# Kernel optimization log

Hardware: AMD Instinct MI355X
Metric: run time of the kernel (lower is better)

Reference implementation:

```python
import jax, jax.numpy as jnp
import numpy as np

BS, S, D, N, E = 16, 8, 10, 32, 300
H, STATE_DIM, MID, OC = 128, 96, 256, 100

def setup_inputs():
    ks = jax.random.split(jax.random.key(0), 24)
    g = lambda i, shape: (0.02 * jax.random.normal(ks[i], shape)).astype(jnp.float32)
    return {
        "stock_news": jax.random.normal(ks[0], (BS, S, D, N, E), dtype=jnp.float32),
        "stock_feats": jax.random.normal(ks[1], (BS, STATE_DIM), dtype=jnp.float32),
        "conv_w3": g(2, (S, OC, E, 3)), "conv_b3": g(3, (S, OC)),
        "conv_w4": g(4, (S, OC, E, 4)), "conv_b4": g(5, (S, OC)),
        "conv_w5": g(6, (S, OC, E, 5)), "conv_b5": g(7, (S, OC)),
        "w_ih": g(8, (S, 4 * H, 3 * OC)), "w_hh": g(9, (S, 4 * H, H)),
        "b_ih": g(10, (S, 4 * H)), "b_hh": g(11, (S, 4 * H)),
        "linX_w": g(12, (S, H, 2 * H)), "linX_b": g(13, (S, H)),
        "linY_w": g(14, (S, 64, H)), "linY_b": g(15, (S, 64)),
        "w1": g(16, (24, STATE_DIM)), "b1": g(17, (24,)),
        "w2": g(18, (16, 24)), "b2": g(19, (16,)),
        "arch_w1": g(20, (MID, 16 + 64 * S)), "arch_b1": g(21, (MID,)),
        "arch_w2": g(22, (S, MID)), "arch_b2": g(23, (S,)),
        "action_var": jnp.full((S,), -0.25, dtype=jnp.float32),
    }

def _conv_maxpool(x, w, b, k):
    # x: [S,B,D,N,E], w: [S,OC,E,k] -> conv1d over news axis then max-pool -> [S,B,D,OC]
    L = x.shape[3] - k + 1
    y = jnp.broadcast_to(b[:, None, None, None, :], (x.shape[0], x.shape[1], x.shape[2], L, w.shape[1]))
    for j in range(k):
        y = y + jnp.einsum('sbdne,soe->sbdno', x[:, :, :, j:j + L, :], w[:, :, :, j])
    return y.max(axis=3)

def _lstm_attn(xs, w_ih, w_hh, b_ih, b_hh):
    # single-stock LSTM (batch_first) + attention from original code; xs: [B,D,I] -> [B,2H]
    pre = jnp.einsum('bdi,gi->dbg', xs, w_ih) + b_ih + b_hh  # [D,B,4H]
    h0 = jnp.zeros((xs.shape[0], w_hh.shape[1]), xs.dtype)
    def step(carry, g_t):
        h, c = carry
        gates = g_t + h @ w_hh.T
        i, f, g, o = jnp.split(gates, 4, axis=-1)  # PyTorch gate order i,f,g,o
        c = jax.nn.sigmoid(f) * c + jax.nn.sigmoid(i) * jnp.tanh(g)
        h = jax.nn.sigmoid(o) * jnp.tanh(c)
        return (h, c), h
    (hn, _), outs = jax.lax.scan(step, (h0, h0), pre)
    outs = outs.transpose(1, 0, 2)  # [B,D,H]
    w = jnp.einsum('bh,bdh->bd', hn, outs)[:, None, :]  # [B,1,D]
    w = jax.nn.softmax(w, axis=1)  # softmax over singleton dim, exactly as torch code (yields ones)
    out = jnp.sum(w.transpose(0, 2, 1) * outs, axis=1)  # [B,H]
    return jnp.concatenate([hn, out], axis=-1)  # [B,2H]

def _forward(stock_news, stock_feats, conv_w3, conv_b3, conv_w4, conv_b4, conv_w5, conv_b5,
             w_ih, w_hh, b_ih, b_hh, linX_w, linX_b, linY_w, linY_b,
             w1, b1, w2, b2, arch_w1, arch_b1, arch_w2, arch_b2, action_var):
    x = stock_news.transpose(1, 0, 2, 3, 4)  # [S,B,D,N,E]
    feats = [_conv_maxpool(x, w, b, k) for (w, b, k) in
             ((conv_w3, conv_b3, 3), (conv_w4, conv_b4, 4), (conv_w5, conv_b5, 5))]
    text = jnp.concatenate(feats, axis=-1)  # [S,B,D,300]
    comb = jax.vmap(_lstm_attn)(text, w_ih, w_hh, b_ih, b_hh)  # [S,B,2H]
    hX = jax.nn.relu(jnp.einsum('sbi,shi->sbh', comb, linX_w) + linX_b[:, None, :])  # dropout is eval-mode identity
    hY = jax.nn.relu(jnp.einsum('sbh,soh->sbo', hX, linY_w) + linY_b[:, None, :])  # [S,B,64]
    stock_text = hY.transpose(1, 0, 2).reshape(stock_news.shape[0], -1)  # [B,S*64]
    f = jax.nn.relu(stock_feats @ w1.T + b1) @ w2.T + b2  # [B,16]
    total = jnp.concatenate([stock_text, f], axis=-1)  # [B,16+64S]
    mu = jnp.tanh(jax.nn.relu(total @ arch_w1.T + arch_b1) @ arch_w2.T + arch_b2)
    return mu, jnp.exp(action_var)

def reference(stock_news, stock_feats, conv_w3, conv_b3, conv_w4, conv_b4, conv_w5, conv_b5,
              w_ih, w_hh, b_ih, b_hh, linX_w, linX_b, linY_w, linY_b,
              w1, b1, w2, b2, arch_w1, arch_b1, arch_w2, arch_b2, action_var):
    return _forward(stock_news, stock_feats, conv_w3, conv_b3, conv_w4, conv_b4, conv_w5, conv_b5,
                    w_ih, w_hh, b_ih, b_hh, linX_w, linX_b, linY_w, linY_b,
                    w1, b1, w2, b2, arch_w1, arch_b1, arch_w2, arch_b2, action_var)
```

## Files before the change

### kernel.cpp

```cpp
#include <hip/hip_runtime.h>
#include <hip/hip_fp8.h>
#include <math.h>

#define S_   8
#define B_   16
#define D_   10
#define N_   32
#define E_   300
#define H_   128
#define G4_  512
#define SDIM_ 96
#define MID_ 256
#define TOT_ 528

#define GP_  514

typedef unsigned short u16;
typedef unsigned int u32;
typedef unsigned char u8;
typedef unsigned long long u64;
typedef __attribute__((ext_vector_type(8))) short short8;
typedef __attribute__((ext_vector_type(4))) float f32x4;

static __device__ __forceinline__ u16 f2bf(float f) {
    unsigned u = __builtin_bit_cast(unsigned, f);
    return (u16)((u + 0x7FFFu + ((u >> 16) & 1u)) >> 16);
}
static __device__ __forceinline__ u8 f2fp8(float f) {
    __hip_fp8_e4m3 t(f);
    return (u8)t.__x;
}

template<int KT>
static __device__ __forceinline__ void fill_row(const float* __restrict__ src,
                                                u8* __restrict__ tilerow, int lane) {
    const float4* s4 = reinterpret_cast<const float4*>(src);
    for (int i4 = lane; i4 < 75 * KT; i4 += 64) {
        float4 v = s4[i4];
        float vv[4] = {v.x, v.y, v.z, v.w};
#pragma unroll
        for (int k = 0; k < 4; ++k) {
            int p = i4 * 4 + k;
            int e = p / KT, tap = p - e * KT;
            tilerow[tap * 300 + e] = f2fp8(vv[k] * 16.0f);
        }
    }
}

__global__ __launch_bounds__(256) void prep(
        const float* __restrict__ w3, const float* __restrict__ b3,
        const float* __restrict__ w4, const float* __restrict__ b4,
        const float* __restrict__ w5, const float* __restrict__ b5,
        const float* __restrict__ w_ih, const float* __restrict__ w_hh,
        const float* __restrict__ lxw, const float* __restrict__ lyw,
        const float* __restrict__ aw1,
        u8* __restrict__ wpack3, u16* __restrict__ wpre2,
        u16* __restrict__ whh_pk, u16* __restrict__ lxw_pk, u16* __restrict__ lyw_pk,
        float* __restrict__ bcomb, float* __restrict__ aw1T) {
    const int blk = blockIdx.x, tid = threadIdx.x;

    if (blk < 640) {
        __shared__ u8 tile4[4][1504];
        const int s = blk / 80, cq = blk % 80;
        const int c0 = cq * 4;
        const int ch4 = tid >> 6, lane = tid & 63;
        for (int i = tid; i < 1504; i += 256)
            reinterpret_cast<u32*>(&tile4[0][0])[i] = 0u;
        __syncthreads();
        const int c = c0 + ch4;
        if (cq < 25)      fill_row<3>(w3 + (size_t)((s * 100 + c      ) * 300) * 3, &tile4[ch4][0], lane);
        else if (cq < 50) fill_row<4>(w4 + (size_t)((s * 100 + c - 100) * 300) * 4, &tile4[ch4][0], lane);
        else if (cq < 75) fill_row<5>(w5 + (size_t)((s * 100 + c - 200) * 300) * 5, &tile4[ch4][0], lane);
        __syncthreads();
        u32* dst0 = reinterpret_cast<u32*>(wpack3) + (size_t)s * 120320;
        const int kss = tid >> 5, m = tid & 31;
        const int ch = m >> 3, b0 = (m & 7) * 4;
#pragma unroll
        for (int ksb = 0; ksb < 6; ++ksb) {
            int ks = ksb * 8 + kss;
            if (ks < 47) {
                int kk = ks * 32 + b0;
                u32 v = (u32)tile4[ch][kk] | ((u32)tile4[ch][kk + 1] << 8)
                      | ((u32)tile4[ch][kk + 2] << 16) | ((u32)tile4[ch][kk + 3] << 24);
                dst0[(size_t)ks * 2560 + cq * 32 + m] = v;
            }
        }
    } else if (blk < 1248) {
        __shared__ u16 tile2[16][320];
        const int ch = tid >> 4, lane = tid & 15;
        u32* dst0; int nks, slab;
        if (blk < 896) {
            int u = blk - 640, s = u >> 5, gg = u & 31;
            int g = gg * 16 + ch;
            const float4* s4 = reinterpret_cast<const float4*>(w_ih + (size_t)(s * 512 + g) * 300);
            for (int i4 = lane; i4 < 75; i4 += 16) {
                float4 v = s4[i4];
                tile2[ch][i4*4+0]=f2bf(v.x); tile2[ch][i4*4+1]=f2bf(v.y);
                tile2[ch][i4*4+2]=f2bf(v.z); tile2[ch][i4*4+3]=f2bf(v.w);
            }
            for (int p = 300 + lane; p < 320; p += 16) tile2[ch][p] = 0;
            dst0 = reinterpret_cast<u32*>(wpre2 + (size_t)s * 163840) + gg * 256;
            nks = 10; slab = 8192;
        } else if (blk < 1152) {
            int u = blk - 896, s = u >> 5, gg = u & 31;
            int g = gg * 16 + ch;
            const float4* s4 = reinterpret_cast<const float4*>(w_hh + (size_t)(s * 512 + g) * 128);
            for (int i4 = lane; i4 < 32; i4 += 16) {
                float4 v = s4[i4];
                tile2[ch][i4*4+0]=f2bf(v.x); tile2[ch][i4*4+1]=f2bf(v.y);
                tile2[ch][i4*4+2]=f2bf(v.z); tile2[ch][i4*4+3]=f2bf(v.w);
            }
            dst0 = reinterpret_cast<u32*>(whh_pk + (size_t)s * 65536) + gg * 256;
            nks = 4; slab = 8192;
        } else if (blk < 1216) {
            int u = blk - 1152, s = u >> 3, gg = u & 7;
            int g = gg * 16 + ch;
            const float4* s4 = reinterpret_cast<const float4*>(lxw + (size_t)(s * 128 + g) * 256);
            for (int i4 = lane; i4 < 64; i4 += 16) {
                float4 v = s4[i4];
                tile2[ch][i4*4+0]=f2bf(v.x); tile2[ch][i4*4+1]=f2bf(v.y);
                tile2[ch][i4*4+2]=f2bf(v.z); tile2[ch][i4*4+3]=f2bf(v.w);
            }
            dst0 = reinterpret_cast<u32*>(lxw_pk + (size_t)s * 32768) + gg * 256;
            nks = 8; slab = 2048;
        } else {
            int u = blk - 1216, s = u >> 2, gg = u & 3;
            int g = gg * 16 + ch;
            const float4* s4 = reinterpret_cast<const float4*>(lyw + (size_t)(s * 64 + g) * 128);
            for (int i4 = lane; i4 < 32; i4 += 16) {
                float4 v = s4[i4];
                tile2[ch][i4*4+0]=f2bf(v.x); tile2[ch][i4*4+1]=f2bf(v.y);
                tile2[ch][i4*4+2]=f2bf(v.z); tile2[ch][i4*4+3]=f2bf(v.w);
            }
            dst0 = reinterpret_cast<u32*>(lyw_pk + (size_t)s * 8192) + gg * 256;
            nks = 4; slab = 1024;
        }
        __syncthreads();
        const int mch = tid >> 4, rem = (tid * 2) & 31;
        for (int ks = 0; ks < nks; ++ks) {
            u32 v = (u32)tile2[mch][ks * 32 + rem] | ((u32)tile2[mch][ks * 32 + rem + 1] << 16);
            dst0[(size_t)ks * slab + tid] = v;
        }
    } else if (blk < 1384) {
        __shared__ float ldsT[32][33];
        int u = blk - 1248;
        int it = u >> 3, jt = u & 7;
        int i0 = it * 32, t0 = jt * 32;
        int ivalid = (i0 + 32 <= 528) ? 32 : (528 - i0);
        const int row = tid >> 3, cf = tid & 7;
        float4 v = make_float4(0.f, 0.f, 0.f, 0.f);
        if (cf * 4 < ivalid)
            v = *reinterpret_cast<const float4*>(aw1 + (size_t)(t0 + row) * 528 + i0 + cf * 4);
        ldsT[cf * 4 + 0][row] = v.x; ldsT[cf * 4 + 1][row] = v.y;
        ldsT[cf * 4 + 2][row] = v.z; ldsT[cf * 4 + 3][row] = v.w;
        __syncthreads();
        if (row < ivalid) {
            float4 w;
            w.x = ldsT[row][cf * 4 + 0]; w.y = ldsT[row][cf * 4 + 1];
            w.z = ldsT[row][cf * 4 + 2]; w.w = ldsT[row][cf * 4 + 3];
            *reinterpret_cast<float4*>(aw1T + (size_t)(i0 + row) * 256 + t0 + cf * 4) = w;
        }
    } else {
        for (int i = tid; i < 2560; i += 256) {
            int c = i % 320, s = i / 320;
            float bv = 0.f;
            if (c < 100)      bv = b3[s*100 + c];
            else if (c < 200) bv = b4[s*100 + c - 100];
            else if (c < 300) bv = b5[s*100 + c - 200];
            bcomb[i] = bv;
        }
    }
}

__global__ __launch_bounds__(512, 1) void conv_mfma(const float* __restrict__ news,
                                                    const u8* __restrict__ wpack3,
                                                    const float* __restrict__ bcomb,
                                                    u16* __restrict__ text_bf) {
    __shared__ u8 xs[5 * 10816];
    float* part = reinterpret_cast<float*>(xs);
    const int tid = threadIdx.x, bid = blockIdx.x;
    const int s = bid & 7, rr_ = bid >> 3, b = rr_ >> 1, half = rr_ & 1;
    const int l = tid & 63, wvi = tid >> 6;
    const int wm = wvi >> 2, wn = wvi & 3;
    const int q = l >> 4, r16 = l & 15;

    const u8* gp[5];
#pragma unroll
    for (int nt = 0; nt < 5; ++nt) {
        int c = wn * 80 + nt * 16 + r16;
        gp[nt] = wpack3 + (size_t)s * 481280 + c * 32 + q * 8;
    }

    u64 bf0[5], bf1[5];
#pragma unroll
    for (int nt = 0; nt < 5; ++nt) bf0[nt] = *reinterpret_cast<const u64*>(gp[nt]);
#pragma unroll
    for (int nt = 0; nt < 5; ++nt) bf1[nt] = *reinterpret_cast<const u64*>(gp[nt] + 10240);

    {
        const float4* xg = reinterpret_cast<const float4*>(
            news + (size_t)((b * 8 + s) * 10 + half * 5) * 9600);
        for (int base = 0; base < 12000; base += 4096) {
            float4 v[8];
#pragma unroll
            for (int j = 0; j < 8; ++j) {
                int idx = base + j * 512 + tid;
                if (idx < 12000) v[j] = xg[idx];
            }
#pragma unroll
            for (int j = 0; j < 8; ++j) {
                int idx = base + j * 512 + tid;
                if (idx < 12000) {
                    int day = idx / 2400, rem = idx - day * 2400;
                    u32 o = (u32)f2fp8(v[j].x) | ((u32)f2fp8(v[j].y) << 8)
                          | ((u32)f2fp8(v[j].z) << 16) | ((u32)f2fp8(v[j].w) << 24);
                    *reinterpret_cast<u32*>(&xs[day * 10816 + rem * 4]) = o;
                }
            }
        }
        for (int i = tid; i < 1520; i += 512) {
            int day = i / 304, p = i - day * 304;
            *reinterpret_cast<u32*>(&xs[day * 10816 + 9600 + p * 4]) = 0u;
        }
    }
    __syncthreads();

    f32x4 acc[5][5];
#pragma unroll
    for (int mt = 0; mt < 5; ++mt)
#pragma unroll
        for (int nt = 0; nt < 5; ++nt) acc[mt][nt] = (f32x4)(0.f);

#define LOADA(dst, ks) do {                                                       \
    _Pragma("unroll")                                                             \
    for (int mt_ = 0; mt_ < 5; ++mt_) {                                           \
        int di_ = wm * 5 + mt_;                                                   \
        int off_ = (di_ >> 1) * 10816 + (((di_ & 1) << 4) + r16) * 300            \
                   + (ks) * 32 + q * 8;                                           \
        u32 lo_ = *reinterpret_cast<const u32*>(&xs[off_]);                       \
        u32 hi_ = *reinterpret_cast<const u32*>(&xs[off_ + 4]);                   \
        dst[mt_] = (u64)lo_ | ((u64)hi_ << 32);                                   \
    } } while (0)

#define MFMAS(bfv, av) do {                                                       \
    _Pragma("unroll")                                                             \
    for (int nt_ = 0; nt_ < 5; ++nt_)                                             \
        _Pragma("unroll")                                                         \
        for (int mt_ = 0; mt_ < 5; ++mt_)                                         \
            acc[mt_][nt_] = __builtin_amdgcn_mfma_f32_16x16x32_fp8_fp8(          \
                (long long)av[mt_], (long long)bfv[nt_], acc[mt_][nt_], 0, 0, 0); \
    } while (0)

    for (int ks = 0; ks < 46; ks += 2) {
        u64 a0[5], a1[5];
        LOADA(a0, ks);
        MFMAS(bf0, a0);
#pragma unroll
        for (int nt = 0; nt < 5; ++nt)
            bf0[nt] = *reinterpret_cast<const u64*>(gp[nt] + (ks + 2) * 10240);

        LOADA(a1, ks + 1);
        MFMAS(bf1, a1);
        if (ks + 3 < 47) {
#pragma unroll
            for (int nt = 0; nt < 5; ++nt)
                bf1[nt] = *reinterpret_cast<const u64*>(gp[nt] + (ks + 3) * 10240);
        }
    }
    {
        u64 a0[5];
        LOADA(a0, 46);
        MFMAS(bf0, a0);
    }
#undef LOADA
#undef MFMAS

    __syncthreads();

#pragma unroll
    for (int mt = 0; mt < 5; ++mt) {
        const int di = wm * 5 + mt;
        const int nwb = (di & 1) << 4;
#pragma unroll
        for (int nt = 0; nt < 5; ++nt) {
            int oc = wn * 80 + nt * 16 + r16;
            int L = (oc < 100) ? 30 : (oc < 200) ? 29 : 28;
            float mx = -3e38f;
#pragma unroll
            for (int rr = 0; rr < 4; ++rr) {
                int nw = nwb + q * 4 + rr;
                if (nw < L) mx = fmaxf(mx, acc[mt][nt][rr]);
            }
            mx = fmaxf(mx, __shfl_xor(mx, 16));
            mx = fmaxf(mx, __shfl_xor(mx, 32));
            if (l < 16) part[di * 320 + wn * 80 + nt * 16 + l] = mx;
        }
    }
    __syncthreads();
    for (int i = tid; i < 1600; i += 512) {
        int day = i / 320, oc = i - day * 320;
        float mx = fmaxf(part[(2 * day) * 320 + oc], part[(2 * day + 1) * 320 + oc]);
        text_bf[((size_t)(s * 16 + b) * 10 + half * 5 + day) * 320 + oc] =
            f2bf(mx * 0.0625f + bcomb[s * 320 + oc]);
    }
}

__global__ __launch_bounds__(256) void lstm_pre_mfma(const u16* __restrict__ text_bf,
                                                     const u16* __restrict__ wpre2,
                                                     const float* __restrict__ b_ih,
                                                     const float* __restrict__ b_hh,
                                                     float* __restrict__ pre) {
    __shared__ u16 as16[16 * 320];
    const int blk = blockIdx.x;
    const int s = blk & 7, rest = blk >> 3;
    const int d = rest % 10, gq = rest / 10;
    const int sd = s * 10 + d;
    const int tid = threadIdx.x, l = tid & 63, w = tid >> 6, q = l >> 4, r16 = l & 15;

    for (int i = tid; i < 640; i += 256) {
        int r = i / 40, c = i % 40;
        *reinterpret_cast<float4*>(as16 + r * 320 + ((c ^ (r & 7)) << 3)) =
            *reinterpret_cast<const float4*>(text_bf + ((size_t)(s * 16 + r) * 10 + d) * 320 + c * 8);
    }
    __syncthreads();

    const u16* gpb[2];
#pragma unroll
    for (int nt = 0; nt < 2; ++nt) {
        int g = gq * 128 + w * 32 + nt * 16 + r16;
        gpb[nt] = wpre2 + (size_t)s * 163840 + g * 32 + q * 8;
    }

    f32x4 acc[2];
#pragma unroll
    for (int nt = 0; nt < 2; ++nt) acc[nt] = (f32x4)(0.f);

    for (int ks = 0; ks < 10; ++ks) {
        short8 a = *reinterpret_cast<const short8*>(
            as16 + r16 * 320 + (((ks * 4 + q) ^ (r16 & 7)) << 3));
#pragma unroll
        for (int nt = 0; nt < 2; ++nt) {
            short8 bf = *reinterpret_cast<const short8*>(gpb[nt] + ks * 16384);
            acc[nt] = __builtin_amdgcn_mfma_f32_16x16x32_bf16(a, bf, acc[nt], 0, 0, 0);
        }
    }

#pragma unroll
    for (int nt = 0; nt < 2; ++nt) {
        int g = gq * 128 + w * 32 + nt * 16 + r16;
        float bias = b_ih[s * G4_ + g] + b_hh[s * G4_ + g];
#pragma unroll
        for (int r = 0; r < 4; ++r) {
            int brow = q * 4 + r;
            pre[((size_t)sd * 16 + brow) * 512 + g] = acc[nt][r] + bias;
        }
    }
}

__global__ __launch_bounds__(512, 1) void stock_tail(const float* __restrict__ pre,
                                                     const u16* __restrict__ whh_pk,
                                                     const u16* __restrict__ lxw_pk,
                                                     const u16* __restrict__ lyw_pk,
                                                     const float* __restrict__ lxb,
                                                     const float* __restrict__ lyb,
                                                     float* __restrict__ total) {
    __shared__ float gates[16 * GP_];
    __shared__ u16 hA[16 * 128];
    __shared__ u16 combA[16 * 256];
    __shared__ u16 hxA[16 * 128];
    const int s = blockIdx.x;
    const int t = threadIdx.x, l = t & 63, wv = t >> 6, q = l >> 4, r16 = l & 15;

    short8 ghr[4][4];
#pragma unroll
    for (int ks2 = 0; ks2 < 4; ++ks2)
#pragma unroll
        for (int nt = 0; nt < 4; ++nt) {
            int g = wv * 64 + nt * 16 + r16;
            ghr[ks2][nt] = *reinterpret_cast<const short8*>(
                whh_pk + (size_t)s * 65536 + ks2 * 16384 + g * 32 + q * 8);
        }

    reinterpret_cast<u64*>(hA)[t] = 0ull;
    float cst[4] = {0.f, 0.f, 0.f, 0.f};
    float hsum[4] = {0.f, 0.f, 0.f, 0.f};

    float pc[16], pn[16];
#pragma unroll
    for (int k = 0; k < 4; ++k) {
        int p = t + 512 * k; int b = p >> 7, h = p & 127;
        const float* base = pre + ((size_t)((s * 10 + 0) * 16 + b)) * 512 + h;
#pragma unroll
        for (int g = 0; g < 4; ++g) pc[k * 4 + g] = base[g * 128];
    }
    __syncthreads();

    for (int d = 0; d < D_; ++d) {
        f32x4 acc[4];
#pragma unroll
        for (int nt = 0; nt < 4; ++nt) acc[nt] = (f32x4)(0.f);
#pragma unroll
        for (int ks2 = 0; ks2 < 4; ++ks2) {
            int gran = (ks2 * 4 + q) ^ (r16 & 7);
            short8 ah = *reinterpret_cast<const short8*>(&hA[r16 * 128 + gran * 8]);
#pragma unroll
            for (int nt = 0; nt < 4; ++nt)
                acc[nt] = __builtin_amdgcn_mfma_f32_16x16x32_bf16(ah, ghr[ks2][nt], acc[nt], 0, 0, 0);
        }
        if (d + 1 < D_) {
#pragma unroll
            for (int k = 0; k < 4; ++k) {
                int p = t + 512 * k; int b = p >> 7, h = p & 127;
                const float* base = pre + ((size_t)((s * 10 + d + 1) * 16 + b)) * 512 + h;
#pragma unroll
                for (int g = 0; g < 4; ++g) pn[k * 4 + g] = base[g * 128];
            }
        }
        __syncthreads();
#pragma unroll
        for (int nt = 0; nt < 4; ++nt) {
            int g = wv * 64 + nt * 16 + r16;
#pragma unroll
            for (int rr = 0; rr < 4; ++rr)
                gates[(q * 4 + rr) * GP_ + g] = acc[nt][rr];
        }
        __syncthreads();
#pragma unroll
        for (int k = 0; k < 4; ++k) {
            int p = t + 512 * k;
            int b = p >> 7, h = p & 127;
            float ig = 1.f / (1.f + expf(-(pc[k*4+0] + gates[b * GP_ + h])));
            float fg = 1.f / (1.f + expf(-(pc[k*4+1] + gates[b * GP_ + 128 + h])));
            float gg = tanhf(pc[k*4+2] + gates[b * GP_ + 256 + h]);
            float og = 1.f / (1.f + expf(-(pc[k*4+3] + gates[b * GP_ + 384 + h])));
            float c = fg * cst[k] + ig * gg;
            cst[k] = c;
            float hv = og * tanhf(c);
            hsum[k] += hv;
            hA[b * 128 + (((h >> 3) ^ (b & 7)) << 3) + (h & 7)] = f2bf(hv);
            if (d == D_ - 1) {
                combA[b * 256 + (((h >> 3) ^ (b & 7)) << 3) + (h & 7)] = f2bf(hv);
                combA[b * 256 + ((((128 + h) >> 3) ^ (b & 7)) << 3) + (h & 7)] = f2bf(hsum[k]);
            }
        }
#pragma unroll
        for (int i = 0; i < 16; ++i) pc[i] = pn[i];
        __syncthreads();
    }

    {
        int col = wv * 16 + r16;
        f32x4 xacc = (f32x4)(lxb[s * H_ + col]);
#pragma unroll
        for (int ks = 0; ks < 8; ++ks) {
            int gran = (ks * 4 + q) ^ (r16 & 7);
            short8 a = *reinterpret_cast<const short8*>(&combA[r16 * 256 + gran * 8]);
            short8 bfr = *reinterpret_cast<const short8*>(
                lxw_pk + (size_t)s * 32768 + ks * 4096 + col * 32 + q * 8);
            xacc = __builtin_amdgcn_mfma_f32_16x16x32_bf16(a, bfr, xacc, 0, 0, 0);
        }
#pragma unroll
        for (int rr = 0; rr < 4; ++rr) {
            int b = q * 4 + rr;
            float v = fmaxf(xacc[rr], 0.f);
            hxA[b * 128 + (((col >> 3) ^ (b & 7)) << 3) + (col & 7)] = f2bf(v);
        }
    }
    __syncthreads();

    if (wv < 4) {
        int col = wv * 16 + r16;
        f32x4 yacc = (f32x4)(lyb[s * 64 + col]);
#pragma unroll
        for (int ks = 0; ks < 4; ++ks) {
            int gran = (ks * 4 + q) ^ (r16 & 7);
            short8 a = *reinterpret_cast<const short8*>(&hxA[r16 * 128 + gran * 8]);
            short8 bfr = *reinterpret_cast<const short8*>(
                lyw_pk + (size_t)s * 8192 + ks * 2048 + col * 32 + q * 8);
            yacc = __builtin_amdgcn_mfma_f32_16x16x32_bf16(a, bfr, yacc, 0, 0, 0);
        }
#pragma unroll
        for (int rr = 0; rr < 4; ++rr) {
            int b = q * 4 + rr;
            total[(size_t)b * 512 + s * 64 + col] = fmaxf(yacc[rr], 0.f);
        }
    }
}

__global__ __launch_bounds__(512) void head_feats(const float* __restrict__ total,
                                                  const float* __restrict__ sf,
                                                  const float* __restrict__ w1, const float* __restrict__ b1,
                                                  const float* __restrict__ w2, const float* __restrict__ b2,
                                                  const float* __restrict__ aw1T, const float* __restrict__ ab1,
                                                  const float* __restrict__ aw2, const float* __restrict__ ab2,
                                                  const float* __restrict__ avar,
                                                  float* __restrict__ out) {
    __shared__ __align__(16) float tr[TOT_];
    __shared__ float hid[MID_];
    __shared__ float h1f[24];
    __shared__ float pA[MID_], pB[MID_];
    const int bb = blockIdx.x, t = threadIdx.x;
    if (t < 128)
        reinterpret_cast<float4*>(tr)[t] = reinterpret_cast<const float4*>(total + (size_t)bb * 512)[t];
    if (t < 24) {
        float acc = b1[t];
        for (int i = 0; i < SDIM_; ++i) acc = fmaf(sf[bb * SDIM_ + i], w1[t * SDIM_ + i], acc);
        h1f[t] = fmaxf(acc, 0.f);
    }
    __syncthreads();
    if (t < 16) {
        float acc = b2[t];
        for (int i = 0; i < 24; ++i) acc = fmaf(h1f[i], w2[t * 24 + i], acc);
        tr[512 + t] = acc;
    }
    __syncthreads();
    {
        const int j = t & 255, hf = t >> 8;
        const int ilo = hf ? 264 : 0, ihi = hf ? 528 : 264;
        const float* wv = aw1T + j;
        float a0 = 0.f, a1 = 0.f, a2 = 0.f, a3 = 0.f;
        for (int i = ilo; i < ihi; i += 4) {
            a0 = fmaf(tr[i + 0], wv[(size_t)(i + 0) * 256], a0);
            a1 = fmaf(tr[i + 1], wv[(size_t)(i + 1) * 256], a1);
            a2 = fmaf(tr[i + 2], wv[(size_t)(i + 2) * 256], a2);
            a3 = fmaf(tr[i + 3], wv[(size_t)(i + 3) * 256], a3);
        }
        float p = (a0 + a1) + (a2 + a3);
        if (hf) pB[j] = p; else pA[j] = p;
    }
    __syncthreads();
    if (t < MID_) hid[t] = fmaxf(pA[t] + pB[t] + ab1[t], 0.f);
    __syncthreads();
    if (t < 8) {
        float acc = ab2[t];
        const float* wv = aw2 + (size_t)t * MID_;
        for (int i = 0; i < MID_; ++i) acc = fmaf(hid[i], wv[i], acc);
        out[bb * 8 + t] = tanhf(acc);
    }
    if (bb == 0 && t >= 8 && t < 16) out[128 + (t - 8)] = expf(avar[t - 8]);
}

extern "C" void kernel_launch(void* const* d_in, const int* in_sizes, int n_in,
                              void* d_out, int out_size, void* d_ws, size_t ws_size,
                              hipStream_t stream) {
    const float* news = (const float*)d_in[0];
    const float* sf   = (const float*)d_in[1];
    const float* w3   = (const float*)d_in[2];  const float* b3 = (const float*)d_in[3];
    const float* w4   = (const float*)d_in[4];  const float* b4 = (const float*)d_in[5];
    const float* w5   = (const float*)d_in[6];  const float* b5 = (const float*)d_in[7];
    const float* w_ih = (const float*)d_in[8];  const float* w_hh = (const float*)d_in[9];
    const float* b_ih = (const float*)d_in[10]; const float* b_hh = (const float*)d_in[11];
    const float* lxw  = (const float*)d_in[12]; const float* lxb = (const float*)d_in[13];
    const float* lyw  = (const float*)d_in[14]; const float* lyb = (const float*)d_in[15];
    const float* w1   = (const float*)d_in[16]; const float* b1 = (const float*)d_in[17];
    const float* w2   = (const float*)d_in[18]; const float* b2 = (const float*)d_in[19];
    const float* aw1  = (const float*)d_in[20]; const float* ab1 = (const float*)d_in[21];
    const float* aw2  = (const float*)d_in[22]; const float* ab2 = (const float*)d_in[23];
    const float* avar = (const float*)d_in[24];

    char* ws = (char*)d_ws;
    u8*    wpack3  = (u8*)ws;
    u16*   wpre2   = (u16*)(ws + 3850240);
    u16*   whh_pk  = (u16*)(ws + 6471680);
    u16*   lxw_pk  = (u16*)(ws + 7520256);
    u16*   lyw_pk  = (u16*)(ws + 8044544);
    float* bcomb   = (float*)(ws + 8175616);
    u16*   text_bf = (u16*)(ws + 8185856);
    float* total   = (float*)(ws + 9005056);
    float* aw1T    = (float*)(ws + 9037824);
    float* pre     = (float*)(ws + 9578496);

    prep<<<1385, 256, 0, stream>>>(w3, b3, w4, b4, w5, b5, w_ih, w_hh, lxw, lyw, aw1,
                                   wpack3, wpre2, whh_pk, lxw_pk, lyw_pk, bcomb, aw1T);
    conv_mfma<<<256, 512, 0, stream>>>(news, wpack3, bcomb, text_bf);
    lstm_pre_mfma<<<320, 256, 0, stream>>>(text_bf, wpre2, b_ih, b_hh, pre);
    stock_tail<<<S_, 512, 0, stream>>>(pre, whh_pk, lxw_pk, lyw_pk, lxb, lyb, total);
    head_feats<<<B_, 512, 0, stream>>>(total, sf, w1, b1, w2, b2, aw1T, ab1, aw2, ab2, avar, (float*)d_out);
}
```

Measured before the change: 111.0 us.

## Split conv output channels across two blocks to double conv grid

The conv kernel now launches 512 blocks instead of 256. Each block computes half of the 320 output channels (160), with the 10 N-tiles spread unevenly across the four column waves (3,3,2,2). This gives more blocks to fill the MI355X's 256 CUs and cuts per-wave accumulator registers. In exchange, each block still loads and converts the full news tile to fp8, so input loading and conversion are duplicated across the pair, and wave work is imbalanced.

After: 111.9 us. No clear change (+0.8%).

```diff
diff --git a/kernel.cpp b/kernel.cpp
--- a/kernel.cpp
+++ b/kernel.cpp
@@ -179,23 +179,29 @@
     __shared__ u8 xs[5 * 10816];
     float* part = reinterpret_cast<float*>(xs);
     const int tid = threadIdx.x, bid = blockIdx.x;
-    const int s = bid & 7, rr_ = bid >> 3, b = rr_ >> 1, half = rr_ & 1;
+    const int s = bid & 7, r_ = bid >> 3;
+    const int b = r_ >> 2, half = (r_ >> 1) & 1, nh = r_ & 1;
     const int l = tid & 63, wvi = tid >> 6;
     const int wm = wvi >> 2, wn = wvi & 3;
     const int q = l >> 4, r16 = l & 15;
-
-    const u8* gp[5];
-#pragma unroll
-    for (int nt = 0; nt < 5; ++nt) {
-        int c = wn * 80 + nt * 16 + r16;
+    const int ntcnt = (wn < 2) ? 3 : 2;
+    const int ntbase = (wn < 2) ? wn * 3 : 6 + (wn - 2) * 2;
+    const int cbase = nh * 160;
+
+    const u8* gp[3];
+#pragma unroll
+    for (int nt = 0; nt < 3; ++nt) {
+        int c = cbase + (ntbase + (nt < ntcnt ? nt : 0)) * 16 + r16;
         gp[nt] = wpack3 + (size_t)s * 481280 + c * 32 + q * 8;
     }
 
-    u64 bf0[5], bf1[5];
-#pragma unroll
-    for (int nt = 0; nt < 5; ++nt) bf0[nt] = *reinterpret_cast<const u64*>(gp[nt]);
-#pragma unroll
-    for (int nt = 0; nt < 5; ++nt) bf1[nt] = *reinterpret_cast<const u64*>(gp[nt] + 10240);
+    u64 bf0[3] = {0, 0, 0}, bf1[3] = {0, 0, 0};
+#pragma unroll
+    for (int nt = 0; nt < 3; ++nt)
+        if (nt < ntcnt) bf0[nt] = *reinterpret_cast<const u64*>(gp[nt]);
+#pragma unroll
+    for (int nt = 0; nt < 3; ++nt)
+        if (nt < ntcnt) bf1[nt] = *reinterpret_cast<const u64*>(gp[nt] + 10240);
 
     {
         const float4* xg = reinterpret_cast<const float4*>(
@@ -225,11 +231,11 @@
     }
     __syncthreads();
 
-    f32x4 acc[5][5];
+    f32x4 acc[5][3];
 #pragma unroll
     for (int mt = 0; mt < 5; ++mt)
 #pragma unroll
-        for (int nt = 0; nt < 5; ++nt) acc[mt][nt] = (f32x4)(0.f);
+        for (int nt = 0; nt < 3; ++nt) acc[mt][nt] = (f32x4)(0.f);
 
 #define LOADA(dst, ks) do {                                                       \
     _Pragma("unroll")                                                             \
@@ -244,11 +250,12 @@
 
 #define MFMAS(bfv, av) do {                                                       \
     _Pragma("unroll")                                                             \
-    for (int nt_ = 0; nt_ < 5; ++nt_)                                             \
-        _Pragma("unroll")                                                         \
-        for (int mt_ = 0; mt_ < 5; ++mt_)                                         \
-            acc[mt_][nt_] = __builtin_amdgcn_mfma_f32_16x16x32_fp8_fp8(          \
-                (long long)av[mt_], (long long)bfv[nt_], acc[mt_][nt_], 0, 0, 0); \
+    for (int nt_ = 0; nt_ < 3; ++nt_)                                             \
+        if (nt_ < ntcnt)                                                          \
+            _Pragma("unroll")                                                     \
+            for (int mt_ = 0; mt_ < 5; ++mt_)                                     \
+                acc[mt_][nt_] = __builtin_amdgcn_mfma_f32_16x16x32_fp8_fp8(      \
+                    (long long)av[mt_], (long long)bfv[nt_], acc[mt_][nt_], 0, 0, 0); \
     } while (0)
 
     for (int ks = 0; ks < 46; ks += 2) {
@@ -256,15 +263,15 @@
         LOADA(a0, ks);
         MFMAS(bf0, a0);
 #pragma unroll
-        for (int nt = 0; nt < 5; ++nt)
-            bf0[nt] = *reinterpret_cast<const u64*>(gp[nt] + (ks + 2) * 10240);
+        for (int nt = 0; nt < 3; ++nt)
+            if (nt < ntcnt) bf0[nt] = *reinterpret_cast<const u64*>(gp[nt] + (ks + 2) * 10240);
 
         LOADA(a1, ks + 1);
         MFMAS(bf1, a1);
         if (ks + 3 < 47) {
 #pragma unroll
-            for (int nt = 0; nt < 5; ++nt)
-                bf1[nt] = *reinterpret_cast<const u64*>(gp[nt] + (ks + 3) * 10240);
+            for (int nt = 0; nt < 3; ++nt)
+                if (nt < ntcnt) bf1[nt] = *reinterpret_cast<const u64*>(gp[nt] + (ks + 3) * 10240);
         }
     }
     {
@@ -282,24 +289,28 @@
         const int di = wm * 5 + mt;
         const int nwb = (di & 1) << 4;
 #pragma unroll
-        for (int nt = 0; nt < 5; ++nt) {
-            int oc = wn * 80 + nt * 16 + r16;
-            int L = (oc < 100) ? 30 : (oc < 200) ? 29 : 28;
-            float mx = -3e38f;
-#pragma unroll
-            for (int rr = 0; rr < 4; ++rr) {
-                int nw = nwb + q * 4 + rr;
-                if (nw < L) mx = fmaxf(mx, acc[mt][nt][rr]);
-            }
-            mx = fmaxf(mx, __shfl_xor(mx, 16));
-            mx = fmaxf(mx, __shfl_xor(mx, 32));
-            if (l < 16) part[di * 320 + wn * 80 + nt * 16 + l] = mx;
-        }
-    }
-    __syncthreads();
-    for (int i = tid; i < 1600; i += 512) {
-        int day = i / 320, oc = i - day * 320;
-        float mx = fmaxf(part[(2 * day) * 320 + oc], part[(2 * day + 1) * 320 + oc]);
+        for (int nt = 0; nt < 3; ++nt) {
+            if (nt < ntcnt) {
+                int ocl = (ntbase + nt) * 16 + r16;
+                int oc = cbase + ocl;
+                int L = (oc < 100) ? 30 : (oc < 200) ? 29 : 28;
+                float mx = -3e38f;
+#pragma unroll
+                for (int rr = 0; rr < 4; ++rr) {
+                    int nw = nwb + q * 4 + rr;
+                    if (nw < L) mx = fmaxf(mx, acc[mt][nt][rr]);
+                }
+                mx = fmaxf(mx, __shfl_xor(mx, 16));
+                mx = fmaxf(mx, __shfl_xor(mx, 32));
+                if (l < 16) part[di * 160 + ocl] = mx;
+            }
+        }
+    }
+    __syncthreads();
+    for (int i = tid; i < 800; i += 512) {
+        int day = i / 160, ocl = i - day * 160;
+        float mx = fmaxf(part[(2 * day) * 160 + ocl], part[(2 * day + 1) * 160 + ocl]);
+        int oc = cbase + ocl;
         text_bf[((size_t)(s * 16 + b) * 10 + half * 5 + day) * 320 + oc] =
             f2bf(mx * 0.0625f + bcomb[s * 320 + oc]);
     }
@@ -572,7 +583,7 @@
 
     prep<<<1385, 256, 0, stream>>>(w3, b3, w4, b4, w5, b5, w_ih, w_hh, lxw, lyw, aw1,
                                    wpack3, wpre2, whh_pk, lxw_pk, lyw_pk, bcomb, aw1T);
-    conv_mfma<<<256, 512, 0, stream>>>(news, wpack3, bcomb, text_bf);
+    conv_mfma<<<512, 512, 0, stream>>>(news, wpack3, bcomb, text_bf);
     lstm_pre_mfma<<<320, 256, 0, stream>>>(text_bf, wpre2, b_ih, b_hh, pre);
     stock_tail<<<S_, 512, 0, stream>>>(pre, whh_pk, lxw_pk, lyw_pk, lxb, lyb, total);
     head_feats<<<B_, 512, 0, stream>>>(total, sf, w1, b1, w2, b2, aw1T, ab1, aw2, ab2, avar, (float*)d_out);
```
